# Optimization experiments

Hardware: AMD Instinct MI355X
Metric: run time of the kernel (lower is better)

Reference implementation:

```python
import jax, jax.numpy as jnp
import numpy as np
import math

WS = 7          # window_size
TOPK = 4        # routed regions
NUM_HEADS = 8   # only used for the scale factor (heads never split in forward)


def _dwconv(v_img, kernel, bias):
    # v_img: (N, ws, ws, C); kernel: (3, 3, 1, C) depthwise (groups=C), padding=1
    out = jax.lax.conv_general_dilated(
        v_img, kernel, window_strides=(1, 1), padding='SAME',
        dimension_numbers=('NHWC', 'HWIO', 'NHWC'),
        feature_group_count=v_img.shape[-1])
    return out + bias


def setup_inputs() -> dict:
    key = jax.random.key(0)
    ks = jax.random.split(key, 12)
    B, H, W, C = 8, 56, 56, 256
    std = 0.02
    return {
        'x': jax.random.normal(ks[0], (B, H, W, C), jnp.float32),
        'w_qkv': jax.random.normal(ks[1], (C, 3 * C), jnp.float32) * std,
        'b_qkv': jnp.zeros((3 * C,), jnp.float32),
        'w_g1': jax.random.normal(ks[2], (C, C // 4), jnp.float32) * std,
        'b_g1': jnp.zeros((C // 4,), jnp.float32),
        'w_g2': jax.random.normal(ks[3], (C // 4, 2), jnp.float32) * std,
        'b_g2': jnp.zeros((2,), jnp.float32),
        'dw_kernel': jax.random.normal(ks[4], (3, 3, 1, C), jnp.float32) * std,
        'dw_bias': jnp.zeros((C,), jnp.float32),
        'w_proj': jax.random.normal(ks[5], (C, C), jnp.float32) * std,
        'b_proj': jnp.zeros((C,), jnp.float32),
    }


def reference(x, w_qkv, b_qkv, w_g1, b_g1, w_g2, b_g2, dw_kernel, dw_bias, w_proj, b_proj):
    B, H, W, C = x.shape
    ws = WS
    nH, nW = H // ws, W // ws      # input chosen divisible by ws (pad path is no-op)
    S, ntok = nH * nW, ws * ws
    t = min(TOPK, S)
    scale = (C // NUM_HEADS) ** (-0.5)

    # window partition: (B, S, ws*ws, C)
    xw = x.reshape(B, nH, ws, nW, ws, C).transpose(0, 1, 3, 2, 4, 5).reshape(B, S, ntok, C)
    x_region = xw.mean(axis=2)                                  # (B, S, C)

    # region-level qkv and routing scores
    qkv_r = (x_region @ w_qkv + b_qkv).reshape(B, S, 3, C)
    q_r, k_r = qkv_r[:, :, 0], qkv_r[:, :, 1]
    A_r = jnp.einsum('bsc,bzc->bsz', q_r, k_r) * scale          # (B, S, S)
    _, topk_idx = jax.lax.top_k(A_r, t)                         # (B, S, t)

    # per-region Gaussian (diagonal covariance) weights over regions
    gp = jax.nn.relu(q_r @ w_g1 + b_g1) @ w_g2 + b_g2           # (B, S, 2)
    sigma = jax.nn.softplus(gp) + 0.5
    s_side = int(round(math.sqrt(S)))
    coords = jnp.arange(s_side, dtype=x.dtype)
    gy, gx = jnp.meshgrid(coords, coords, indexing='ij')
    mu = jnp.stack([gx.ravel(), gy.ravel()], axis=-1)           # (S, 2) as (x, y)
    d = mu[None, :, :] - mu[:, None, :]                         # (S, S, 2): mu_j - mu_i
    z = (d[..., 0][None] / sigma[..., 0][:, :, None]) ** 2 \
        + (d[..., 1][None] / sigma[..., 1][:, :, None]) ** 2    # (B, S, S)
    gauss = jnp.exp(-0.5 * z)
    gauss = gauss / (gauss.sum(-1, keepdims=True) + 1e-6)
    gwt = jnp.take_along_axis(gauss, topk_idx, axis=2)          # (B, S, t)

    # token-level qkv within windows
    qkv = (xw @ w_qkv + b_qkv).reshape(B, S, ntok, 3, C)
    q, k, v = qkv[..., 0, :], qkv[..., 1, :], qkv[..., 2, :]    # (B, S, ntok, C)

    # gather routed windows and reweight by Gaussian
    gather = jax.vmap(lambda a, i: a[i])                        # over batch
    k_g = (gather(k, topk_idx) * gwt[..., None, None]).reshape(B, S, t * ntok, C)
    v_g = (gather(v, topk_idx) * gwt[..., None, None]).reshape(B, S, t * ntok, C)

    attn = jax.nn.softmax(jnp.einsum('bswc,bskc->bswk', q, k_g) * scale, axis=-1)
    out = jnp.einsum('bswk,bskc->bswc', attn, v_g)              # (B, S, ntok, C)

    # depthwise-conv branch on v
    vdw = _dwconv(v.reshape(B * S, ws, ws, C), dw_kernel, dw_bias).reshape(B, S, ntok, C)
    out = out + vdw

    # window merge + output projection
    out = out.reshape(B, nH, nW, ws, ws, C).transpose(0, 1, 3, 2, 4, 5).reshape(B, H, W, C)
    return out @ w_proj + b_proj
```

## Files before the change

### kernel.cpp

```cpp
#include <hip/hip_runtime.h>
#include <math.h>

#define SCALE 0.17677669529663687f

typedef short short8 __attribute__((ext_vector_type(8)));
typedef float f32x4 __attribute__((ext_vector_type(4)));

__device__ __forceinline__ int token_row_addr(int m) {
    int b = m / 3136;
    int rem = m - b * 3136;
    int s = rem / 49;
    int tok = rem - s * 49;
    int h = (s >> 3) * 7 + tok / 7;
    int w = (s & 7) * 7 + (tok % 7);
    return (b * 56 + h) * 56 + w;
}

__device__ __forceinline__ void split2(float x, unsigned short& h, unsigned short& l) {
    unsigned int u = __float_as_uint(x);
    h = (unsigned short)(u >> 16);
    float hf = __uint_as_float(u & 0xFFFF0000u);
    l = (unsigned short)(__float_as_uint(x - hf) >> 16);
}

__device__ __forceinline__ void gload16(const unsigned short* g, unsigned short* l) {
    __builtin_amdgcn_global_load_lds(
        (const __attribute__((address_space(1))) unsigned int*)g,
        (__attribute__((address_space(3))) unsigned int*)l, 16, 0, 0);
}

__global__ void k_cvt_x(const float* __restrict__ x, unsigned short* __restrict__ xhi,
                        unsigned short* __restrict__ xlo) {
    int m = blockIdx.x;
    int k = threadIdx.x;
    float v = x[(size_t)token_row_addr(m) * 256 + k];
    unsigned short h, l;
    split2(v, h, l);
    xhi[(size_t)m * 256 + k] = h;
    xlo[(size_t)m * 256 + k] = l;
}

__global__ void k_cvt_w(const float* __restrict__ w, int ncols,
                        unsigned short* __restrict__ whi, unsigned short* __restrict__ wlo) {
    int n = blockIdx.x;
    int k = threadIdx.x;
    float v = w[(size_t)k * ncols + n];
    unsigned short h, l;
    split2(v, h, l);
    whi[(size_t)n * 256 + k] = h;
    wlo[(size_t)n * 256 + k] = l;
}

__global__ void k_region_mean(const float* __restrict__ x, float* __restrict__ xr) {
    int blk = blockIdx.x;
    int b = blk >> 6, s = blk & 63;
    int c = threadIdx.x;
    int hy0 = (s >> 3) * 7, wx0 = (s & 7) * 7;
    const float* xb = x + ((size_t)b * 56 * 56) * 256 + c;
    float sum = 0.f;
#pragma unroll 1
    for (int t = 0; t < 49; ++t) {
        int h = hy0 + t / 7, w = wx0 + (t % 7);
        sum += xb[(size_t)(h * 56 + w) * 256];
    }
    xr[(size_t)blk * 256 + c] = sum * (1.0f / 49.0f);
}

__global__ void k_region_qkv(const float* __restrict__ xr, const float* __restrict__ wqkv,
                             const float* __restrict__ bqkv, float* __restrict__ qkvr) {
    __shared__ float xs[256];
    int blk = blockIdx.x;
    int t = threadIdx.x;
    xs[t] = xr[(size_t)blk * 256 + t];
    __syncthreads();
    float a0 = 0.f, a1 = 0.f, a2 = 0.f;
#pragma unroll 4
    for (int k = 0; k < 256; ++k) {
        float xv = xs[k];
        const float* wrow = wqkv + (size_t)k * 768;
        a0 += xv * wrow[t];
        a1 += xv * wrow[t + 256];
        a2 += xv * wrow[t + 512];
    }
    float* o = qkvr + (size_t)blk * 768;
    o[t]       = a0 + bqkv[t];
    o[t + 256] = a1 + bqkv[t + 256];
    o[t + 512] = a2 + bqkv[t + 512];
}

__global__ void k_gating(const float* __restrict__ qkvr, const float* __restrict__ wg1,
                         const float* __restrict__ bg1, const float* __restrict__ wg2,
                         const float* __restrict__ bg2, float* __restrict__ sig) {
    __shared__ float hs[64];
    int blk = blockIdx.x;
    int j = threadIdx.x;
    const float* qr = qkvr + (size_t)blk * 768;
    float acc = bg1[j];
#pragma unroll 4
    for (int k = 0; k < 256; ++k) acc += qr[k] * wg1[(size_t)k * 64 + j];
    hs[j] = fmaxf(acc, 0.f);
    __syncthreads();
    if (j < 2) {
        float gp = bg2[j];
#pragma unroll 1
        for (int m = 0; m < 64; ++m) gp += hs[m] * wg2[m * 2 + j];
        float sp = fmaxf(gp, 0.f) + log1pf(expf(-fabsf(gp)));
        sig[blk * 2 + j] = sp + 0.5f;
    }
}

__global__ void k_topk_gauss(const float* __restrict__ qkvr, const float* __restrict__ sig,
                             int* __restrict__ topk, float* __restrict__ gwt) {
    __shared__ float A[64];
    __shared__ float G[64];
    __shared__ int idxs[4];
    __shared__ float gsum_s;
    int blk = blockIdx.x;
    int b = blk >> 6, s = blk & 63;
    int z = threadIdx.x;
    const float* qr = qkvr + (size_t)blk * 768;
    const float* kr = qkvr + (size_t)(b * 64 + z) * 768 + 256;
    float acc = 0.f;
#pragma unroll 4
    for (int k = 0; k < 256; k += 4) {
        float4 q4 = *(const float4*)(qr + k);
        float4 k4 = *(const float4*)(kr + k);
        acc += q4.x * k4.x + q4.y * k4.y + q4.z * k4.z + q4.w * k4.w;
    }
    A[z] = acc * SCALE;
    float s0 = sig[blk * 2 + 0], s1 = sig[blk * 2 + 1];
    float dx = (float)((z & 7) - (s & 7));
    float dy = (float)((z >> 3) - (s >> 3));
    float t0 = dx / s0, t1 = dy / s1;
    float zz = t0 * t0 + t1 * t1;
    G[z] = expf(-0.5f * zz);
    __syncthreads();
    if (z == 0) {
        float gs = 0.f;
        for (int m = 0; m < 64; ++m) gs += G[m];
        gsum_s = gs + 1e-6f;
        for (int it = 0; it < 4; ++it) {
            int best = 0;
            float bv = A[0];
            for (int m = 1; m < 64; ++m) {
                if (A[m] > bv) { bv = A[m]; best = m; }
            }
            idxs[it] = best;
            A[best] = -3.0e38f;
        }
    }
    __syncthreads();
    if (z < 4) {
        int id = idxs[z];
        topk[blk * 4 + z] = id;
        gwt[blk * 4 + z] = G[id] / gsum_s;
    }
}

__global__ __launch_bounds__(256) void k_mm_qkv(
    const unsigned short* __restrict__ xhi, const unsigned short* __restrict__ xlo,
    const unsigned short* __restrict__ whi, const unsigned short* __restrict__ wlo,
    const float* __restrict__ bqkv,
    float* __restrict__ Q, float* __restrict__ Kb, float* __restrict__ V) {
    __shared__ __align__(16) unsigned short Ah[4096];
    __shared__ __align__(16) unsigned short Al[4096];
    __shared__ __align__(16) unsigned short Bh[4096];
    __shared__ __align__(16) unsigned short Bl[4096];
    int tid = threadIdx.x;
    int ln = tid & 63, wv = tid >> 6;
    int m0 = blockIdx.y * 128, n0 = blockIdx.x * 128;
    int mrow = (wv >> 1) * 64, ncol = (wv & 1) * 64;

    int lrow = ln >> 2, lseg = (ln & 3) * 8;
    const unsigned short* gA0 = xhi + (size_t)(m0 + wv * 32 + lrow) * 256 + lseg;
    const unsigned short* gA1 = gA0 + 16 * 256;
    const unsigned short* gAl0 = xlo + (size_t)(m0 + wv * 32 + lrow) * 256 + lseg;
    const unsigned short* gAl1 = gAl0 + 16 * 256;
    const unsigned short* gB0 = whi + (size_t)(n0 + wv * 32 + lrow) * 256 + lseg;
    const unsigned short* gB1 = gB0 + 16 * 256;
    const unsigned short* gBl0 = wlo + (size_t)(n0 + wv * 32 + lrow) * 256 + lseg;
    const unsigned short* gBl1 = gBl0 + 16 * 256;
    unsigned short* lA0 = &Ah[(wv * 32) * 32];
    unsigned short* lA1 = &Ah[(wv * 32 + 16) * 32];
    unsigned short* lAl0 = &Al[(wv * 32) * 32];
    unsigned short* lAl1 = &Al[(wv * 32 + 16) * 32];
    unsigned short* lB0 = &Bh[(wv * 32) * 32];
    unsigned short* lB1 = &Bh[(wv * 32 + 16) * 32];
    unsigned short* lBl0 = &Bl[(wv * 32) * 32];
    unsigned short* lBl1 = &Bl[(wv * 32 + 16) * 32];

    int fm = ln & 15, fq = (ln >> 4) * 8;
    f32x4 acc[4][4];
#pragma unroll
    for (int i = 0; i < 4; ++i)
#pragma unroll
        for (int j = 0; j < 4; ++j) acc[i][j] = (f32x4){0.f, 0.f, 0.f, 0.f};

#pragma unroll 1
    for (int kc = 0; kc < 8; ++kc) {
        if (kc) __syncthreads();
        gload16(gA0, lA0); gload16(gA1, lA1);
        gload16(gAl0, lAl0); gload16(gAl1, lAl1);
        gload16(gB0, lB0); gload16(gB1, lB1);
        gload16(gBl0, lBl0); gload16(gBl1, lBl1);
        gA0 += 32; gA1 += 32; gAl0 += 32; gAl1 += 32;
        gB0 += 32; gB1 += 32; gBl0 += 32; gBl1 += 32;
        __syncthreads();

        short8 ah[4], bh[4], xx[4];
#pragma unroll
        for (int mi = 0; mi < 4; ++mi)
            ah[mi] = *(const short8*)&Ah[(mrow + mi * 16 + fm) * 32 + fq];
#pragma unroll
        for (int ni = 0; ni < 4; ++ni)
            bh[ni] = *(const short8*)&Bh[(ncol + ni * 16 + fm) * 32 + fq];
#pragma unroll
        for (int mi = 0; mi < 4; ++mi)
#pragma unroll
            for (int ni = 0; ni < 4; ++ni)
                acc[mi][ni] = __builtin_amdgcn_mfma_f32_16x16x32_bf16(ah[mi], bh[ni], acc[mi][ni], 0, 0, 0);
#pragma unroll
        for (int mi = 0; mi < 4; ++mi)
            xx[mi] = *(const short8*)&Al[(mrow + mi * 16 + fm) * 32 + fq];
#pragma unroll
        for (int mi = 0; mi < 4; ++mi)
#pragma unroll
            for (int ni = 0; ni < 4; ++ni)
                acc[mi][ni] = __builtin_amdgcn_mfma_f32_16x16x32_bf16(xx[mi], bh[ni], acc[mi][ni], 0, 0, 0);
#pragma unroll
        for (int ni = 0; ni < 4; ++ni)
            xx[ni] = *(const short8*)&Bl[(ncol + ni * 16 + fm) * 32 + fq];
#pragma unroll
        for (int mi = 0; mi < 4; ++mi)
#pragma unroll
            for (int ni = 0; ni < 4; ++ni)
                acc[mi][ni] = __builtin_amdgcn_mfma_f32_16x16x32_bf16(ah[mi], xx[ni], acc[mi][ni], 0, 0, 0);
    }

    int obuf = n0 >> 8;
    float* dst = (obuf == 0) ? Q : (obuf == 1 ? Kb : V);
    int cb = (n0 & 255) + ncol;
    int qrow = (ln >> 4) * 4;
#pragma unroll
    for (int ni = 0; ni < 4; ++ni) {
        int col = cb + ni * 16 + fm;
        float bias = bqkv[n0 + ncol + ni * 16 + fm];
#pragma unroll
        for (int mi = 0; mi < 4; ++mi) {
#pragma unroll
            for (int r = 0; r < 4; ++r) {
                int m = m0 + mrow + mi * 16 + qrow + r;
                dst[(size_t)m * 256 + col] = acc[mi][ni][r] + bias;
            }
        }
    }
}

__global__ __launch_bounds__(256) void k_attn_logits_sm(
    const float* __restrict__ Q, const float* __restrict__ Kb,
    const int* __restrict__ topk, const float* __restrict__ gwt,
    float* __restrict__ Pt) {
    __shared__ float Ls[49][209];
    __shared__ float As[16][68];
    __shared__ float Bs[16][68];
    __shared__ float red[49][4];
    __shared__ float rowm[49];
    __shared__ float rinv[49];
    int win = blockIdx.x;
    int b = win >> 6;
    int tid = threadIdx.x;
    int ty = tid >> 4, tx = tid & 15;
    int ar = tid >> 2, ak = (tid & 3) * 4;
    int aw = ar < 49 ? ar : 48;
    const float* qbase = Q + ((size_t)win * 49 + aw) * 256 + ak;

#pragma unroll 1
    for (int r = 0; r < 4; ++r) {
        int reg = topk[win * 4 + r];
        float sg = SCALE * gwt[win * 4 + r];
        int btok = ar < 49 ? ar : 48;
        const float* kbase = Kb + ((size_t)(b * 64 + reg) * 49 + btok) * 256 + ak;
        float acc[4][4] = {};
#pragma unroll 1
        for (int kc = 0; kc < 256; kc += 16) {
            float4 a4 = *(const float4*)(qbase + kc);
            float4 b4 = {0.f, 0.f, 0.f, 0.f};
            if (tid < 208) b4 = *(const float4*)(kbase + kc);
            __syncthreads();
            As[ak + 0][ar] = a4.x;
            As[ak + 1][ar] = a4.y;
            As[ak + 2][ar] = a4.z;
            As[ak + 3][ar] = a4.w;
            if (tid < 208) {
                Bs[ak + 0][ar] = b4.x;
                Bs[ak + 1][ar] = b4.y;
                Bs[ak + 2][ar] = b4.z;
                Bs[ak + 3][ar] = b4.w;
            }
            __syncthreads();
#pragma unroll
            for (int kk = 0; kk < 16; ++kk) {
                float4 av4 = *(const float4*)&As[kk][ty * 4];
                float4 bv4 = *(const float4*)&Bs[kk][tx * 4];
                float av[4] = {av4.x, av4.y, av4.z, av4.w};
                float bv[4] = {bv4.x, bv4.y, bv4.z, bv4.w};
#pragma unroll
                for (int i = 0; i < 4; ++i)
#pragma unroll
                    for (int j = 0; j < 4; ++j) acc[i][j] += av[i] * bv[j];
            }
        }
        if (tx < 13) {
#pragma unroll
            for (int i = 0; i < 4; ++i) {
                int w = ty * 4 + i;
                if (w < 49) {
#pragma unroll
                    for (int j = 0; j < 4; ++j) {
                        int tok = tx * 4 + j;
                        Ls[w][r * 52 + tok] = (tok < 49) ? acc[i][j] * sg : -3.0e38f;
                    }
                }
            }
        }
    }
    __syncthreads();

    int sw = tid >> 2, sp = tid & 3;
    if (tid < 196) {
        float m = -3.0e38f;
        for (int j = sp; j < 208; j += 4) m = fmaxf(m, Ls[sw][j]);
        red[sw][sp] = m;
    }
    __syncthreads();
    if (tid < 49)
        rowm[tid] = fmaxf(fmaxf(red[tid][0], red[tid][1]), fmaxf(red[tid][2], red[tid][3]));
    __syncthreads();
    if (tid < 196) {
        float m = rowm[sw], s = 0.f;
        for (int j = sp; j < 208; j += 4) {
            float e = expf(Ls[sw][j] - m);
            Ls[sw][j] = e;
            s += e;
        }
        red[sw][sp] = s;
    }
    __syncthreads();
    if (tid < 49)
        rinv[tid] = 1.0f / (red[tid][0] + red[tid][1] + red[tid][2] + red[tid][3]);
    __syncthreads();

    int w2 = tid & 63, jg = tid >> 6;
    if (w2 < 52) {
        float rv = (w2 < 49) ? rinv[w2] : 0.f;
#pragma unroll 1
        for (int r = 0; r < 4; ++r) {
            float gw = gwt[win * 4 + r];
            float* pt = Pt + ((size_t)win * 208 + r * 52) * 52 + w2;
#pragma unroll 1
            for (int j = jg; j < 52; j += 4) {
                float v = 0.f;
                if (w2 < 49) v = Ls[w2][r * 52 + j] * rv * gw;
                pt[(size_t)j * 52] = v;
            }
        }
    }
}

__global__ __launch_bounds__(256) void k_attn_pv(
    const float* __restrict__ Pt, const float* __restrict__ V,
    const int* __restrict__ topk, const float* __restrict__ dwk,
    const float* __restrict__ dwb, unsigned short* __restrict__ atthi,
    unsigned short* __restrict__ attlo) {
    __shared__ float As[16][68];
    __shared__ float Vs[16][68];
    int bx = blockIdx.x;
    int win = bx >> 2, cq = bx & 3, c0 = cq * 64;
    int b = win >> 6;
    int tid = threadIdx.x;
    int jr = tid >> 4, q4 = (tid & 15) * 4;
    int ty = tid >> 4, tx = tid & 15;
    int r0 = topk[win * 4 + 0], r1 = topk[win * 4 + 1];
    int r2 = topk[win * 4 + 2], r3 = topk[win * 4 + 3];

    float acc[4][4] = {};
#pragma unroll 1
    for (int jt = 0; jt < 208; jt += 16) {
        int j = jt + jr;
        float4 a4 = {0.f, 0.f, 0.f, 0.f};
        if (q4 < 52) a4 = *(const float4*)(Pt + ((size_t)win * 208 + j) * 52 + q4);
        int r = (j >= 156) ? 3 : (j >= 104) ? 2 : (j >= 52) ? 1 : 0;
        int reg = (r == 0) ? r0 : (r == 1) ? r1 : (r == 2) ? r2 : r3;
        int tok = j - r * 52;
        tok = tok < 49 ? tok : 48;
        float4 v4 = *(const float4*)(V + ((size_t)(b * 64 + reg) * 49 + tok) * 256 + c0 + q4);
        __syncthreads();
        if (q4 < 52) *(float4*)&As[jr][q4] = a4;
        *(float4*)&Vs[jr][q4] = v4;
        __syncthreads();
#pragma unroll
        for (int kk = 0; kk < 16; ++kk) {
            float4 av4 = *(const float4*)&As[kk][ty * 4];
            float4 bv4 = *(const float4*)&Vs[kk][tx * 4];
            float av[4] = {av4.x, av4.y, av4.z, av4.w};
            float bv[4] = {bv4.x, bv4.y, bv4.z, bv4.w};
#pragma unroll
            for (int i = 0; i < 4; ++i)
#pragma unroll
                for (int j2 = 0; j2 < 4; ++j2) acc[i][j2] += av[i] * bv[j2];
        }
    }

    if (ty < 13) {
        const float* vw = V + (size_t)win * 49 * 256 + c0 + tx * 4;
        const float* dk = dwk + c0 + tx * 4;
        float4 db4 = *(const float4*)(dwb + c0 + tx * 4);
#pragma unroll
        for (int i = 0; i < 4; ++i) {
            int w = ty * 4 + i;
            if (w < 49) {
                int py = w / 7, px = w - py * 7;
                float4 vd = db4;
#pragma unroll
                for (int dy = 0; dy < 3; ++dy) {
                    int yy = py + dy - 1;
                    if (yy < 0 || yy > 6) continue;
#pragma unroll
                    for (int dx = 0; dx < 3; ++dx) {
                        int xx = px + dx - 1;
                        if (xx < 0 || xx > 6) continue;
                        float4 vv = *(const float4*)(vw + (size_t)(yy * 7 + xx) * 256);
                        float4 kk4 = *(const float4*)(dk + (size_t)(dy * 3 + dx) * 256);
                        vd.x += vv.x * kk4.x;
                        vd.y += vv.y * kk4.y;
                        vd.z += vv.z * kk4.z;
                        vd.w += vv.w * kk4.w;
                    }
                }
                float o[4] = {acc[i][0] + vd.x, acc[i][1] + vd.y,
                              acc[i][2] + vd.z, acc[i][3] + vd.w};
                ushort4 oh, ol;
                split2(o[0], oh.x, ol.x);
                split2(o[1], oh.y, ol.y);
                split2(o[2], oh.z, ol.z);
                split2(o[3], oh.w, ol.w);
                size_t idx = ((size_t)win * 49 + w) * 256 + c0 + tx * 4;
                *(ushort4*)(atthi + idx) = oh;
                *(ushort4*)(attlo + idx) = ol;
            }
        }
    }
}

__global__ __launch_bounds__(256) void k_mm_proj(
    const unsigned short* __restrict__ ahi, const unsigned short* __restrict__ alo,
    const unsigned short* __restrict__ whi, const unsigned short* __restrict__ wlo,
    const float* __restrict__ bp, float* __restrict__ out) {
    __shared__ __align__(16) unsigned short Ah[4096];
    __shared__ __align__(16) unsigned short Al[4096];
    __shared__ __align__(16) unsigned short Bh[4096];
    __shared__ __align__(16) unsigned short Bl[4096];
    int tid = threadIdx.x;
    int ln = tid & 63, wv = tid >> 6;
    int m0 = blockIdx.y * 128, n0 = blockIdx.x * 128;
    int mrow = (wv >> 1) * 64, ncol = (wv & 1) * 64;

    int lrow = ln >> 2, lseg = (ln & 3) * 8;
    const unsigned short* gA0 = ahi + (size_t)(m0 + wv * 32 + lrow) * 256 + lseg;
    const unsigned short* gA1 = gA0 + 16 * 256;
    const unsigned short* gAl0 = alo + (size_t)(m0 + wv * 32 + lrow) * 256 + lseg;
    const unsigned short* gAl1 = gAl0 + 16 * 256;
    const unsigned short* gB0 = whi + (size_t)(n0 + wv * 32 + lrow) * 256 + lseg;
    const unsigned short* gB1 = gB0 + 16 * 256;
    const unsigned short* gBl0 = wlo + (size_t)(n0 + wv * 32 + lrow) * 256 + lseg;
    const unsigned short* gBl1 = gBl0 + 16 * 256;
    unsigned short* lA0 = &Ah[(wv * 32) * 32];
    unsigned short* lA1 = &Ah[(wv * 32 + 16) * 32];
    unsigned short* lAl0 = &Al[(wv * 32) * 32];
    unsigned short* lAl1 = &Al[(wv * 32 + 16) * 32];
    unsigned short* lB0 = &Bh[(wv * 32) * 32];
    unsigned short* lB1 = &Bh[(wv * 32 + 16) * 32];
    unsigned short* lBl0 = &Bl[(wv * 32) * 32];
    unsigned short* lBl1 = &Bl[(wv * 32 + 16) * 32];

    int fm = ln & 15, fq = (ln >> 4) * 8;
    f32x4 acc[4][4];
#pragma unroll
    for (int i = 0; i < 4; ++i)
#pragma unroll
        for (int j = 0; j < 4; ++j) acc[i][j] = (f32x4){0.f, 0.f, 0.f, 0.f};

#pragma unroll 1
    for (int kc = 0; kc < 8; ++kc) {
        if (kc) __syncthreads();
        gload16(gA0, lA0); gload16(gA1, lA1);
        gload16(gAl0, lAl0); gload16(gAl1, lAl1);
        gload16(gB0, lB0); gload16(gB1, lB1);
        gload16(gBl0, lBl0); gload16(gBl1, lBl1);
        gA0 += 32; gA1 += 32; gAl0 += 32; gAl1 += 32;
        gB0 += 32; gB1 += 32; gBl0 += 32; gBl1 += 32;
        __syncthreads();

        short8 ah[4], bh[4], xx[4];
#pragma unroll
        for (int mi = 0; mi < 4; ++mi)
            ah[mi] = *(const short8*)&Ah[(mrow + mi * 16 + fm) * 32 + fq];
#pragma unroll
        for (int ni = 0; ni < 4; ++ni)
            bh[ni] = *(const short8*)&Bh[(ncol + ni * 16 + fm) * 32 + fq];
#pragma unroll
        for (int mi = 0; mi < 4; ++mi)
#pragma unroll
            for (int ni = 0; ni < 4; ++ni)
                acc[mi][ni] = __builtin_amdgcn_mfma_f32_16x16x32_bf16(ah[mi], bh[ni], acc[mi][ni], 0, 0, 0);
#pragma unroll
        for (int mi = 0; mi < 4; ++mi)
            xx[mi] = *(const short8*)&Al[(mrow + mi * 16 + fm) * 32 + fq];
#pragma unroll
        for (int mi = 0; mi < 4; ++mi)
#pragma unroll
            for (int ni = 0; ni < 4; ++ni)
                acc[mi][ni] = __builtin_amdgcn_mfma_f32_16x16x32_bf16(xx[mi], bh[ni], acc[mi][ni], 0, 0, 0);
#pragma unroll
        for (int ni = 0; ni < 4; ++ni)
            xx[ni] = *(const short8*)&Bl[(ncol + ni * 16 + fm) * 32 + fq];
#pragma unroll
        for (int mi = 0; mi < 4; ++mi)
#pragma unroll
            for (int ni = 0; ni < 4; ++ni)
                acc[mi][ni] = __builtin_amdgcn_mfma_f32_16x16x32_bf16(ah[mi], xx[ni], acc[mi][ni], 0, 0, 0);
    }

    int qrow = (ln >> 4) * 4;
#pragma unroll
    for (int mi = 0; mi < 4; ++mi) {
#pragma unroll
        for (int r = 0; r < 4; ++r) {
            int m = m0 + mrow + mi * 16 + qrow + r;
            size_t orow = (size_t)token_row_addr(m);
#pragma unroll
            for (int ni = 0; ni < 4; ++ni) {
                int col = n0 + ncol + ni * 16 + fm;
                out[orow * 256 + col] = acc[mi][ni][r] + bp[col];
            }
        }
    }
}

extern "C" void kernel_launch(void* const* d_in, const int* in_sizes, int n_in,
                              void* d_out, int out_size, void* d_ws, size_t ws_size,
                              hipStream_t stream) {
    const float* x    = (const float*)d_in[0];
    const float* wqkv = (const float*)d_in[1];
    const float* bqkv = (const float*)d_in[2];
    const float* wg1  = (const float*)d_in[3];
    const float* bg1  = (const float*)d_in[4];
    const float* wg2  = (const float*)d_in[5];
    const float* bg2  = (const float*)d_in[6];
    const float* dwk  = (const float*)d_in[7];
    const float* dwb  = (const float*)d_in[8];
    const float* wp   = (const float*)d_in[9];
    const float* bp   = (const float*)d_in[10];
    float* out = (float*)d_out;
    float* ws = (float*)d_ws;

    const size_t NTOT = (size_t)25088 * 256;
    const size_t PTSZ = (size_t)512 * 208 * 52;
    float* Qf  = ws;
    float* Kf  = Qf + NTOT;
    float* Vf  = Kf + NTOT;
    float* Pt  = Vf + NTOT;
    unsigned short* XH = (unsigned short*)(Pt + PTSZ);
    unsigned short* XL = XH + NTOT;
    unsigned short* WQH = XL + NTOT;
    unsigned short* WQL = WQH + 768 * 256;
    unsigned short* WPH = WQL + 768 * 256;
    unsigned short* WPL = WPH + 256 * 256;
    float* XR   = (float*)(WPL + 256 * 256);
    float* QKVR = XR + 512 * 256;
    float* SIG  = QKVR + 512 * 768;
    float* GWT  = SIG + 1024;
    int*   TOPK = (int*)(GWT + 2048);

    hipLaunchKernelGGL(k_cvt_x, dim3(25088), dim3(256), 0, stream, x, XH, XL);
    hipLaunchKernelGGL(k_cvt_w, dim3(768), dim3(256), 0, stream, wqkv, 768, WQH, WQL);
    hipLaunchKernelGGL(k_cvt_w, dim3(256), dim3(256), 0, stream, wp, 256, WPH, WPL);
    hipLaunchKernelGGL(k_region_mean, dim3(512), dim3(256), 0, stream, x, XR);
    hipLaunchKernelGGL(k_region_qkv, dim3(512), dim3(256), 0, stream, XR, wqkv, bqkv, QKVR);
    hipLaunchKernelGGL(k_gating, dim3(512), dim3(64), 0, stream, QKVR, wg1, bg1, wg2, bg2, SIG);
    hipLaunchKernelGGL(k_topk_gauss, dim3(512), dim3(64), 0, stream, QKVR, SIG, TOPK, GWT);
    hipLaunchKernelGGL(k_mm_qkv, dim3(6, 196), dim3(256), 0, stream,
                       XH, XL, WQH, WQL, bqkv, Qf, Kf, Vf);
    hipLaunchKernelGGL(k_attn_logits_sm, dim3(512), dim3(256), 0, stream,
                       Qf, Kf, TOPK, GWT, Pt);
    hipLaunchKernelGGL(k_attn_pv, dim3(2048), dim3(256), 0, stream,
                       Pt, Vf, TOPK, dwk, dwb, XH , XL );
    hipLaunchKernelGGL(k_mm_proj, dim3(2, 196), dim3(256), 0, stream,
                       XH, XL, WPH, WPL, bp, out);
}
```

Before: 397.2 us.

## Move window attention logits and PV onto bf16x3 MFMA with transposed V layout

The QKV GEMM now writes Q, K and V as hi/lo bf16 pairs instead of fp32, with V stored transposed per window and padded to 64 tokens. The attention logits and P·V products now use split-bf16 (three-product) MFMA instead of FP32 SIMT loops through shared memory. The probability matrix is emitted as padded bf16 hi/lo. The depthwise conv reads the transposed bf16 V. This targets the SIMT FMA cost and the fp32 bandwidth of the attention stage. In exchange it adds narrow scattered 2-byte stores, and it reads the unwritten V padding columns, which are multiplied by zero but could poison results if the workspace holds NaN patterns.

```diff
diff --git a/kernel.cpp b/kernel.cpp
--- a/kernel.cpp
+++ b/kernel.cpp
@@ -21,6 +21,10 @@
     h = (unsigned short)(u >> 16);
     float hf = __uint_as_float(u & 0xFFFF0000u);
     l = (unsigned short)(__float_as_uint(x - hf) >> 16);
+}
+
+__device__ __forceinline__ float b2f(unsigned short u) {
+    return __uint_as_float(((unsigned int)u) << 16);
 }
 
 __device__ __forceinline__ void gload16(const unsigned short* g, unsigned short* l) {
@@ -161,7 +165,9 @@
     const unsigned short* __restrict__ xhi, const unsigned short* __restrict__ xlo,
     const unsigned short* __restrict__ whi, const unsigned short* __restrict__ wlo,
     const float* __restrict__ bqkv,
-    float* __restrict__ Q, float* __restrict__ Kb, float* __restrict__ V) {
+    unsigned short* __restrict__ Qh, unsigned short* __restrict__ Ql,
+    unsigned short* __restrict__ Kh, unsigned short* __restrict__ Kl,
+    unsigned short* __restrict__ Vth, unsigned short* __restrict__ Vtl) {
     __shared__ __align__(16) unsigned short Ah[4096];
     __shared__ __align__(16) unsigned short Al[4096];
     __shared__ __align__(16) unsigned short Bh[4096];
@@ -237,89 +243,112 @@
                 acc[mi][ni] = __builtin_amdgcn_mfma_f32_16x16x32_bf16(ah[mi], xx[ni], acc[mi][ni], 0, 0, 0);
     }
 
-    int obuf = n0 >> 8;
-    float* dst = (obuf == 0) ? Q : (obuf == 1 ? Kb : V);
-    int cb = (n0 & 255) + ncol;
+    int nb = n0 >> 7;
     int qrow = (ln >> 4) * 4;
 #pragma unroll
     for (int ni = 0; ni < 4; ++ni) {
-        int col = cb + ni * 16 + fm;
+        int col = (n0 & 255) + ncol + ni * 16 + fm;
         float bias = bqkv[n0 + ncol + ni * 16 + fm];
 #pragma unroll
         for (int mi = 0; mi < 4; ++mi) {
 #pragma unroll
             for (int r = 0; r < 4; ++r) {
                 int m = m0 + mrow + mi * 16 + qrow + r;
-                dst[(size_t)m * 256 + col] = acc[mi][ni][r] + bias;
-            }
-        }
-    }
-}
-
-__global__ __launch_bounds__(256) void k_attn_logits_sm(
-    const float* __restrict__ Q, const float* __restrict__ Kb,
+                float v = acc[mi][ni][r] + bias;
+                unsigned short h, l;
+                split2(v, h, l);
+                if (nb < 2) {
+                    size_t idx = (size_t)m * 256 + col;
+                    Qh[idx] = h; Ql[idx] = l;
+                } else if (nb < 4) {
+                    size_t idx = (size_t)m * 256 + col;
+                    Kh[idx] = h; Kl[idx] = l;
+                } else {
+                    unsigned int wn = (unsigned int)m / 49u;
+                    int tok = m - (int)wn * 49;
+                    size_t idx = (size_t)wn * 16384 + (size_t)col * 64 + tok;
+                    Vth[idx] = h; Vtl[idx] = l;
+                }
+            }
+        }
+    }
+}
+
+__global__ __launch_bounds__(256) void k_attn_logits_mfma(
+    const unsigned short* __restrict__ Qh, const unsigned short* __restrict__ Ql,
+    const unsigned short* __restrict__ Kh, const unsigned short* __restrict__ Kl,
     const int* __restrict__ topk, const float* __restrict__ gwt,
-    float* __restrict__ Pt) {
+    unsigned short* __restrict__ Pth, unsigned short* __restrict__ Ptl) {
     __shared__ float Ls[49][209];
-    __shared__ float As[16][68];
-    __shared__ float Bs[16][68];
     __shared__ float red[49][4];
     __shared__ float rowm[49];
-    __shared__ float rinv[49];
+    __shared__ float rinv49[49];
+    __shared__ float gws[4];
     int win = blockIdx.x;
     int b = win >> 6;
     int tid = threadIdx.x;
-    int ty = tid >> 4, tx = tid & 15;
-    int ar = tid >> 2, ak = (tid & 3) * 4;
-    int aw = ar < 49 ? ar : 48;
-    const float* qbase = Q + ((size_t)win * 49 + aw) * 256 + ak;
-
-#pragma unroll 1
-    for (int r = 0; r < 4; ++r) {
-        int reg = topk[win * 4 + r];
-        float sg = SCALE * gwt[win * 4 + r];
-        int btok = ar < 49 ? ar : 48;
-        const float* kbase = Kb + ((size_t)(b * 64 + reg) * 49 + btok) * 256 + ak;
-        float acc[4][4] = {};
-#pragma unroll 1
-        for (int kc = 0; kc < 256; kc += 16) {
-            float4 a4 = *(const float4*)(qbase + kc);
-            float4 b4 = {0.f, 0.f, 0.f, 0.f};
-            if (tid < 208) b4 = *(const float4*)(kbase + kc);
-            __syncthreads();
-            As[ak + 0][ar] = a4.x;
-            As[ak + 1][ar] = a4.y;
-            As[ak + 2][ar] = a4.z;
-            As[ak + 3][ar] = a4.w;
-            if (tid < 208) {
-                Bs[ak + 0][ar] = b4.x;
-                Bs[ak + 1][ar] = b4.y;
-                Bs[ak + 2][ar] = b4.z;
-                Bs[ak + 3][ar] = b4.w;
-            }
-            __syncthreads();
-#pragma unroll
-            for (int kk = 0; kk < 16; ++kk) {
-                float4 av4 = *(const float4*)&As[kk][ty * 4];
-                float4 bv4 = *(const float4*)&Bs[kk][tx * 4];
-                float av[4] = {av4.x, av4.y, av4.z, av4.w};
-                float bv[4] = {bv4.x, bv4.y, bv4.z, bv4.w};
-#pragma unroll
-                for (int i = 0; i < 4; ++i)
-#pragma unroll
-                    for (int j = 0; j < 4; ++j) acc[i][j] += av[i] * bv[j];
-            }
-        }
-        if (tx < 13) {
-#pragma unroll
-            for (int i = 0; i < 4; ++i) {
-                int w = ty * 4 + i;
-                if (w < 49) {
-#pragma unroll
-                    for (int j = 0; j < 4; ++j) {
-                        int tok = tx * 4 + j;
-                        Ls[w][r * 52 + tok] = (tok < 49) ? acc[i][j] * sg : -3.0e38f;
-                    }
+    int ln = tid & 63, wv = tid >> 6;
+    int fm = ln & 15, fq = (ln >> 4) * 8;
+
+    for (int idx = tid; idx < 49 * 12; idx += 256) {
+        int w = idx / 12, t = idx - w * 12;
+        int r = t >> 2, p = t & 3;
+        (void)r; (void)p;
+    }
+    for (int idx = tid; idx < 588; idx += 256) {
+        int w = idx / 12, t = idx - w * 12;
+        int r = t / 3, p = t - r * 3;
+        Ls[w][r * 52 + 49 + p] = -3.0e38f;
+    }
+    if (tid < 4) gws[tid] = gwt[win * 4 + tid];
+
+    int reg = topk[win * 4 + wv];
+    float sg = SCALE * gwt[win * 4 + wv];
+    const size_t qbase = (size_t)win * 49 * 256;
+    const size_t kbase = (size_t)(b * 64 + reg) * 49 * 256;
+
+    f32x4 acc[4][4];
+#pragma unroll
+    for (int i = 0; i < 4; ++i)
+#pragma unroll
+        for (int j = 0; j < 4; ++j) acc[i][j] = (f32x4){0.f, 0.f, 0.f, 0.f};
+
+#pragma unroll 1
+    for (int kc = 0; kc < 256; kc += 32) {
+        short8 ah[4], al[4], bh[4], bl[4];
+#pragma unroll
+        for (int mi = 0; mi < 4; ++mi) {
+            size_t o = qbase + (size_t)(mi * 16 + fm) * 256 + kc + fq;
+            ah[mi] = *(const short8*)&Qh[o];
+            al[mi] = *(const short8*)&Ql[o];
+        }
+#pragma unroll
+        for (int ni = 0; ni < 4; ++ni) {
+            size_t o = kbase + (size_t)(ni * 16 + fm) * 256 + kc + fq;
+            bh[ni] = *(const short8*)&Kh[o];
+            bl[ni] = *(const short8*)&Kl[o];
+        }
+#pragma unroll
+        for (int mi = 0; mi < 4; ++mi)
+#pragma unroll
+            for (int ni = 0; ni < 4; ++ni) {
+                acc[mi][ni] = __builtin_amdgcn_mfma_f32_16x16x32_bf16(ah[mi], bh[ni], acc[mi][ni], 0, 0, 0);
+                acc[mi][ni] = __builtin_amdgcn_mfma_f32_16x16x32_bf16(al[mi], bh[ni], acc[mi][ni], 0, 0, 0);
+                acc[mi][ni] = __builtin_amdgcn_mfma_f32_16x16x32_bf16(ah[mi], bl[ni], acc[mi][ni], 0, 0, 0);
+            }
+    }
+
+    int qrow = (ln >> 4) * 4;
+#pragma unroll
+    for (int mi = 0; mi < 4; ++mi) {
+#pragma unroll
+        for (int r = 0; r < 4; ++r) {
+            int w = mi * 16 + qrow + r;
+            if (w < 49) {
+#pragma unroll
+                for (int ni = 0; ni < 4; ++ni) {
+                    int tok = ni * 16 + fm;
+                    if (tok < 49) Ls[w][wv * 52 + tok] = acc[mi][ni][r] * sg;
                 }
             }
         }
@@ -347,106 +376,116 @@
     }
     __syncthreads();
     if (tid < 49)
-        rinv[tid] = 1.0f / (red[tid][0] + red[tid][1] + red[tid][2] + red[tid][3]);
-    __syncthreads();
-
-    int w2 = tid & 63, jg = tid >> 6;
-    if (w2 < 52) {
-        float rv = (w2 < 49) ? rinv[w2] : 0.f;
-#pragma unroll 1
-        for (int r = 0; r < 4; ++r) {
-            float gw = gwt[win * 4 + r];
-            float* pt = Pt + ((size_t)win * 208 + r * 52) * 52 + w2;
-#pragma unroll 1
-            for (int j = jg; j < 52; j += 4) {
-                float v = 0.f;
-                if (w2 < 49) v = Ls[w2][r * 52 + j] * rv * gw;
-                pt[(size_t)j * 52] = v;
-            }
-        }
-    }
-}
-
-__global__ __launch_bounds__(256) void k_attn_pv(
-    const float* __restrict__ Pt, const float* __restrict__ V,
+        rinv49[tid] = 1.0f / (red[tid][0] + red[tid][1] + red[tid][2] + red[tid][3]);
+    __syncthreads();
+
+    {
+        int w = tid >> 2, r = tid & 3;
+        float rv = (w < 49) ? rinv49[w] * gws[r] : 0.f;
+        size_t base = (size_t)win * 16384 + (size_t)w * 256 + r * 64;
+#pragma unroll 1
+        for (int tok = 0; tok < 64; ++tok) {
+            float v = 0.f;
+            if (w < 49 && tok < 49) v = Ls[w][r * 52 + tok] * rv;
+            unsigned short h, l;
+            split2(v, h, l);
+            Pth[base + tok] = h;
+            Ptl[base + tok] = l;
+        }
+    }
+}
+
+__global__ __launch_bounds__(256) void k_attn_pv_mfma(
+    const unsigned short* __restrict__ Pth, const unsigned short* __restrict__ Ptl,
+    const unsigned short* __restrict__ Vth, const unsigned short* __restrict__ Vtl,
     const int* __restrict__ topk, const float* __restrict__ dwk,
-    const float* __restrict__ dwb, unsigned short* __restrict__ atthi,
-    unsigned short* __restrict__ attlo) {
-    __shared__ float As[16][68];
-    __shared__ float Vs[16][68];
-    int bx = blockIdx.x;
-    int win = bx >> 2, cq = bx & 3, c0 = cq * 64;
+    const float* __restrict__ dwb, unsigned short* __restrict__ atth,
+    unsigned short* __restrict__ attl) {
+    int win = blockIdx.x;
     int b = win >> 6;
     int tid = threadIdx.x;
-    int jr = tid >> 4, q4 = (tid & 15) * 4;
-    int ty = tid >> 4, tx = tid & 15;
-    int r0 = topk[win * 4 + 0], r1 = topk[win * 4 + 1];
-    int r2 = topk[win * 4 + 2], r3 = topk[win * 4 + 3];
-
-    float acc[4][4] = {};
-#pragma unroll 1
-    for (int jt = 0; jt < 208; jt += 16) {
-        int j = jt + jr;
-        float4 a4 = {0.f, 0.f, 0.f, 0.f};
-        if (q4 < 52) a4 = *(const float4*)(Pt + ((size_t)win * 208 + j) * 52 + q4);
-        int r = (j >= 156) ? 3 : (j >= 104) ? 2 : (j >= 52) ? 1 : 0;
-        int reg = (r == 0) ? r0 : (r == 1) ? r1 : (r == 2) ? r2 : r3;
-        int tok = j - r * 52;
-        tok = tok < 49 ? tok : 48;
-        float4 v4 = *(const float4*)(V + ((size_t)(b * 64 + reg) * 49 + tok) * 256 + c0 + q4);
-        __syncthreads();
-        if (q4 < 52) *(float4*)&As[jr][q4] = a4;
-        *(float4*)&Vs[jr][q4] = v4;
-        __syncthreads();
-#pragma unroll
-        for (int kk = 0; kk < 16; ++kk) {
-            float4 av4 = *(const float4*)&As[kk][ty * 4];
-            float4 bv4 = *(const float4*)&Vs[kk][tx * 4];
-            float av[4] = {av4.x, av4.y, av4.z, av4.w};
-            float bv[4] = {bv4.x, bv4.y, bv4.z, bv4.w};
-#pragma unroll
-            for (int i = 0; i < 4; ++i)
-#pragma unroll
-                for (int j2 = 0; j2 < 4; ++j2) acc[i][j2] += av[i] * bv[j2];
-        }
-    }
-
-    if (ty < 13) {
-        const float* vw = V + (size_t)win * 49 * 256 + c0 + tx * 4;
-        const float* dk = dwk + c0 + tx * 4;
-        float4 db4 = *(const float4*)(dwb + c0 + tx * 4);
-#pragma unroll
-        for (int i = 0; i < 4; ++i) {
-            int w = ty * 4 + i;
-            if (w < 49) {
-                int py = w / 7, px = w - py * 7;
-                float4 vd = db4;
-#pragma unroll
-                for (int dy = 0; dy < 3; ++dy) {
-                    int yy = py + dy - 1;
-                    if (yy < 0 || yy > 6) continue;
-#pragma unroll
-                    for (int dx = 0; dx < 3; ++dx) {
-                        int xx = px + dx - 1;
-                        if (xx < 0 || xx > 6) continue;
-                        float4 vv = *(const float4*)(vw + (size_t)(yy * 7 + xx) * 256);
-                        float4 kk4 = *(const float4*)(dk + (size_t)(dy * 3 + dx) * 256);
-                        vd.x += vv.x * kk4.x;
-                        vd.y += vv.y * kk4.y;
-                        vd.z += vv.z * kk4.z;
-                        vd.w += vv.w * kk4.w;
+    int ln = tid & 63, wv = tid >> 6;
+    int fm = ln & 15, fq = (ln >> 4) * 8;
+    int ncol = wv * 64;
+    size_t pbase = (size_t)win * 16384;
+
+    f32x4 acc[4][4];
+#pragma unroll
+    for (int i = 0; i < 4; ++i)
+#pragma unroll
+        for (int j = 0; j < 4; ++j) acc[i][j] = (f32x4){0.f, 0.f, 0.f, 0.f};
+
+#pragma unroll 1
+    for (int r = 0; r < 4; ++r) {
+        int reg = topk[win * 4 + r];
+        size_t vbase = (size_t)(b * 64 + reg) * 16384;
+#pragma unroll
+        for (int half = 0; half < 2; ++half) {
+            int kc = r * 64 + half * 32;
+            int vt = half * 32;
+            short8 ah[4], al[4], bh[4], bl[4];
+#pragma unroll
+            for (int mi = 0; mi < 4; ++mi) {
+                size_t o = pbase + (size_t)(mi * 16 + fm) * 256 + kc + fq;
+                ah[mi] = *(const short8*)&Pth[o];
+                al[mi] = *(const short8*)&Ptl[o];
+            }
+#pragma unroll
+            for (int ni = 0; ni < 4; ++ni) {
+                size_t o = vbase + (size_t)(ncol + ni * 16 + fm) * 64 + vt + fq;
+                bh[ni] = *(const short8*)&Vth[o];
+                bl[ni] = *(const short8*)&Vtl[o];
+            }
+#pragma unroll
+            for (int mi = 0; mi < 4; ++mi)
+#pragma unroll
+                for (int ni = 0; ni < 4; ++ni) {
+                    acc[mi][ni] = __builtin_amdgcn_mfma_f32_16x16x32_bf16(ah[mi], bh[ni], acc[mi][ni], 0, 0, 0);
+                    acc[mi][ni] = __builtin_amdgcn_mfma_f32_16x16x32_bf16(al[mi], bh[ni], acc[mi][ni], 0, 0, 0);
+                    acc[mi][ni] = __builtin_amdgcn_mfma_f32_16x16x32_bf16(ah[mi], bl[ni], acc[mi][ni], 0, 0, 0);
+                }
+        }
+    }
+
+    int qrow = (ln >> 4) * 4;
+    size_t vown = (size_t)win * 16384;
+#pragma unroll 1
+    for (int ni = 0; ni < 4; ++ni) {
+        int c = ncol + ni * 16 + fm;
+        float dk[9];
+#pragma unroll
+        for (int t = 0; t < 9; ++t) dk[t] = dwk[(size_t)t * 256 + c];
+        float db = dwb[c];
+        const unsigned short* vh = Vth + vown + (size_t)c * 64;
+        const unsigned short* vl = Vtl + vown + (size_t)c * 64;
+#pragma unroll
+        for (int mi = 0; mi < 4; ++mi) {
+#pragma unroll
+            for (int rr = 0; rr < 4; ++rr) {
+                int w = mi * 16 + qrow + rr;
+                if (w < 49) {
+                    int py = w / 7, px = w - py * 7;
+                    float vd = db;
+#pragma unroll
+                    for (int dy = 0; dy < 3; ++dy) {
+                        int yy = py + dy - 1;
+                        if (yy < 0 || yy > 6) continue;
+#pragma unroll
+                        for (int dx = 0; dx < 3; ++dx) {
+                            int xx = px + dx - 1;
+                            if (xx < 0 || xx > 6) continue;
+                            int nt = yy * 7 + xx;
+                            float v = b2f(vh[nt]) + b2f(vl[nt]);
+                            vd += v * dk[dy * 3 + dx];
+                        }
                     }
+                    float o = acc[mi][ni][rr] + vd;
+                    unsigned short h, l;
+                    split2(o, h, l);
+                    size_t idx = ((size_t)win * 49 + w) * 256 + c;
+                    atth[idx] = h;
+                    attl[idx] = l;
                 }
-                float o[4] = {acc[i][0] + vd.x, acc[i][1] + vd.y,
-                              acc[i][2] + vd.z, acc[i][3] + vd.w};
-                ushort4 oh, ol;
-                split2(o[0], oh.x, ol.x);
-                split2(o[1], oh.y, ol.y);
-                split2(o[2], oh.z, ol.z);
-                split2(o[3], oh.w, ol.w);
-                size_t idx = ((size_t)win * 49 + w) * 256 + c0 + tx * 4;
-                *(ushort4*)(atthi + idx) = oh;
-                *(ushort4*)(attlo + idx) = ol;
             }
         }
     }
@@ -562,16 +601,19 @@
     const float* wp   = (const float*)d_in[9];
     const float* bp   = (const float*)d_in[10];
     float* out = (float*)d_out;
-    float* ws = (float*)d_ws;
 
     const size_t NTOT = (size_t)25088 * 256;
-    const size_t PTSZ = (size_t)512 * 208 * 52;
-    float* Qf  = ws;
-    float* Kf  = Qf + NTOT;
-    float* Vf  = Kf + NTOT;
-    float* Pt  = Vf + NTOT;
-    unsigned short* XH = (unsigned short*)(Pt + PTSZ);
-    unsigned short* XL = XH + NTOT;
+    const size_t VTSZ = (size_t)512 * 256 * 64;
+    unsigned short* Qh  = (unsigned short*)d_ws;
+    unsigned short* Ql  = Qh + NTOT;
+    unsigned short* Kh  = Ql + NTOT;
+    unsigned short* Kl  = Kh + NTOT;
+    unsigned short* Vth = Kl + NTOT;
+    unsigned short* Vtl = Vth + VTSZ;
+    unsigned short* Pth = Vtl + VTSZ;
+    unsigned short* Ptl = Pth + VTSZ;
+    unsigned short* XH  = Ptl + VTSZ;
+    unsigned short* XL  = XH + NTOT;
     unsigned short* WQH = XL + NTOT;
     unsigned short* WQL = WQH + 768 * 256;
     unsigned short* WPH = WQL + 768 * 256;
@@ -590,11 +632,11 @@
     hipLaunchKernelGGL(k_gating, dim3(512), dim3(64), 0, stream, QKVR, wg1, bg1, wg2, bg2, SIG);
     hipLaunchKernelGGL(k_topk_gauss, dim3(512), dim3(64), 0, stream, QKVR, SIG, TOPK, GWT);
     hipLaunchKernelGGL(k_mm_qkv, dim3(6, 196), dim3(256), 0, stream,
-                       XH, XL, WQH, WQL, bqkv, Qf, Kf, Vf);
-    hipLaunchKernelGGL(k_attn_logits_sm, dim3(512), dim3(256), 0, stream,
-                       Qf, Kf, TOPK, GWT, Pt);
-    hipLaunchKernelGGL(k_attn_pv, dim3(2048), dim3(256), 0, stream,
-                       Pt, Vf, TOPK, dwk, dwb, XH , XL );
+                       XH, XL, WQH, WQL, bqkv, Qh, Ql, Kh, Kl, Vth, Vtl);
+    hipLaunchKernelGGL(k_attn_logits_mfma, dim3(512), dim3(256), 0, stream,
+                       Qh, Ql, Kh, Kl, TOPK, GWT, Pth, Ptl);
+    hipLaunchKernelGGL(k_attn_pv_mfma, dim3(512), dim3(256), 0, stream,
+                       Pth, Ptl, Vth, Vtl, TOPK, dwk, dwb, XH, XL);
     hipLaunchKernelGGL(k_mm_proj, dim3(2, 196), dim3(256), 0, stream,
                        XH, XL, WPH, WPL, bp, out);
 }
```

Result: slower. 735.3 us (+85.1%).
